# Kernel tuning notes

Measured on AMD Instinct MI355X. Metric: run time of the kernel, lower is better.

The kernel has to match this reference:

```python
import jax, jax.numpy as jnp
import numpy as np

N_HEAD = 16


def setup_inputs() -> dict:
    key = jax.random.key(0)
    ks = jax.random.split(key, 11)
    B, T, D = 8, 448, 1024
    init = 0.02
    x = jax.random.normal(ks[0], (B, T, D), dtype=jnp.float32)
    k_cache = jax.random.normal(ks[1], (B, T, D), dtype=jnp.float32)
    v_cache = jax.random.normal(ks[2], (B, T, D), dtype=jnp.float32)
    # Whisper-style additive causal mask: 0 on/below diagonal, large negative above
    mask = jnp.triu(jnp.full((T, T), -1e9, dtype=jnp.float32), k=1)
    Wq = jax.random.normal(ks[3], (D, D), dtype=jnp.float32) * init
    bq = jax.random.normal(ks[4], (D,), dtype=jnp.float32) * init
    Wk = jax.random.normal(ks[5], (D, D), dtype=jnp.float32) * init  # key proj has no bias
    Wv = jax.random.normal(ks[6], (D, D), dtype=jnp.float32) * init
    bv = jax.random.normal(ks[7], (D,), dtype=jnp.float32) * init
    Wo = jax.random.normal(ks[8], (D, D), dtype=jnp.float32) * init
    bo = jax.random.normal(ks[9], (D,), dtype=jnp.float32) * init
    return {"x": x, "k_cache": k_cache, "v_cache": v_cache, "mask": mask,
            "Wq": Wq, "bq": bq, "Wk": Wk, "Wv": Wv, "bv": bv, "Wo": Wo, "bo": bo}


def reference(x, k_cache, v_cache, mask, Wq, bq, Wk, Wv, bv, Wo, bo):
    # QKV projections (key has no bias, as in Whisper)
    q = x @ Wq + bq
    k = x @ Wk
    v = x @ Wv + bv
    # In-place KV cache append: write new keys/values into the tail of the cache
    T_new = k.shape[1]
    k_cache = k_cache.at[:, -T_new:, :].set(k)
    v_cache = v_cache.at[:, -T_new:, :].set(v)

    B, T, D = q.shape
    H = N_HEAD
    dh = D // H
    scale = dh ** (-0.25)  # applied to BOTH q and k

    qh = (q * scale).reshape(B, T, H, dh).transpose(0, 2, 1, 3)           # [B,H,T,dh]
    kh = (k_cache * scale).reshape(B, k_cache.shape[1], H, dh).transpose(0, 2, 1, 3)
    vh = v_cache.reshape(B, v_cache.shape[1], H, dh).transpose(0, 2, 1, 3)

    qk = jnp.einsum('bhqd,bhkd->bhqk', qh, kh) + mask[:T, :T]             # [B,H,T,Tc]
    qk = qk.astype(jnp.float32)  # upcast for softmax, matching original
    w = jax.nn.softmax(qk, axis=-1).astype(q.dtype)

    out = jnp.einsum('bhqk,bhkd->bhqd', w, vh)                            # [B,H,T,dh]
    out = out.transpose(0, 2, 1, 3).reshape(B, T, D)
    return out @ Wo + bo, k_cache, v_cache
```

## Files before the change

kernel.cpp:

```cpp
#include <hip/hip_runtime.h>
#include <hip/hip_bf16.h>
#include <math.h>

#define B 8
#define T 448
#define D 1024
#define H 16
#define DH 64
#define M (B*T)

typedef short short8 __attribute__((ext_vector_type(8)));
typedef float floatx4 __attribute__((ext_vector_type(4)));
typedef unsigned short u16;

__device__ __forceinline__ u16 f2bf(float f) {
    union { float f; unsigned u; } v; v.f = f;
    unsigned r = v.u + 0x7FFF + ((v.u >> 16) & 1);
    return (u16)(r >> 16);
}

__device__ __forceinline__ void gload16(const void* gptr, void* lptr) {
    __builtin_amdgcn_global_load_lds(
        (const __attribute__((address_space(1))) void*)gptr,
        (__attribute__((address_space(3))) void*)lptr, 16, 0, 0);
}

__global__ __launch_bounds__(256) void xconv(const float* __restrict__ x, u16* __restrict__ xb) {
    const int i = blockIdx.x * 256 + threadIdx.x;
    float4 v = ((const float4*)x)[i];
    ushort4 o;
    o.x = f2bf(v.x); o.y = f2bf(v.y); o.z = f2bf(v.z); o.w = f2bf(v.w);
    ((ushort4*)xb)[i] = o;
}

__global__ __launch_bounds__(256) void wconv4(
    const float* __restrict__ Wq, const float* __restrict__ Wk,
    const float* __restrict__ Wv, const float* __restrict__ Wo,
    u16* __restrict__ wt)
{
    __shared__ float tile[64][65];
    const int z = blockIdx.z;
    const float* W = (z == 0) ? Wq : (z == 1) ? Wk : (z == 2) ? Wv : Wo;
    u16* Wt = wt + (size_t)z * D * D;
    const int k0 = blockIdx.y * 64, n0 = blockIdx.x * 64;
    const int tr = threadIdx.x >> 4, tc = threadIdx.x & 15;
    #pragma unroll
    for (int i = 0; i < 4; ++i) {
        float4 v = *(const float4*)(W + (size_t)(k0 + tr + 16 * i) * D + n0 + tc * 4);
        tile[tr + 16 * i][tc * 4 + 0] = v.x;
        tile[tr + 16 * i][tc * 4 + 1] = v.y;
        tile[tr + 16 * i][tc * 4 + 2] = v.z;
        tile[tr + 16 * i][tc * 4 + 3] = v.w;
    }
    __syncthreads();
    #pragma unroll
    for (int i = 0; i < 4; ++i) {
        const int n = tr + 16 * i;
        ushort4 o;
        o.x = f2bf(tile[tc * 4 + 0][n]);
        o.y = f2bf(tile[tc * 4 + 1][n]);
        o.z = f2bf(tile[tc * 4 + 2][n]);
        o.w = f2bf(tile[tc * 4 + 3][n]);
        *(ushort4*)(Wt + (size_t)(n0 + n) * D + k0 + tc * 4) = o;
    }
}

__global__ __launch_bounds__(256) void gemm128(
    const u16* __restrict__ A, const u16* __restrict__ Bt, int mode,
    const float* __restrict__ bq, const float* __restrict__ bv,
    u16* __restrict__ qkvb, float* __restrict__ kout, float* __restrict__ vout,
    u16* __restrict__ vbT,
    const float* __restrict__ bo, float* __restrict__ outp)
{
    __shared__ u16 As[2][128][32];
    __shared__ u16 Bs[2][128][32];
    const int m0 = blockIdx.y * 128;
    const int n0 = blockIdx.x * 128;
    const int tid = threadIdx.x;
    const int wave = tid >> 6, lane = tid & 63;
    const int wy = wave >> 1, wx = wave & 1;
    const int lrow = lane & 15, lquad = lane >> 4;

    floatx4 acc[4][4];
    #pragma unroll
    for (int i = 0; i < 4; ++i)
        #pragma unroll
        for (int j = 0; j < 4; ++j)
            acc[i][j] = (floatx4){0.f, 0.f, 0.f, 0.f};

    const u16* agp0 = A + (size_t)(m0 + (tid >> 2)) * 1024 + (tid & 3) * 8;
    const u16* agp1 = agp0 + (size_t)64 * 1024;
    const u16* bgp0 = Bt + (size_t)(n0 + (tid >> 2)) * 1024 + (tid & 3) * 8;
    const u16* bgp1 = bgp0 + (size_t)64 * 1024;
    char* lA[2] = { (char*)&As[0][0][0] + wave * 1024, (char*)&As[1][0][0] + wave * 1024 };
    char* lB[2] = { (char*)&Bs[0][0][0] + wave * 1024, (char*)&Bs[1][0][0] + wave * 1024 };

    gload16(agp0, lA[0]);
    gload16(agp1, lA[0] + 4096);
    gload16(bgp0, lB[0]);
    gload16(bgp1, lB[0] + 4096);

    for (int it = 0; it < 32; ++it) {
        const int cur = it & 1;
        __syncthreads();
        if (it < 31) {
            const int k = (it + 1) * 32;
            const int nx = cur ^ 1;
            gload16(agp0 + k, lA[nx]);
            gload16(agp1 + k, lA[nx] + 4096);
            gload16(bgp0 + k, lB[nx]);
            gload16(bgp1 + k, lB[nx] + 4096);
        }
        short8 af[4], bfr[4];
        #pragma unroll
        for (int i = 0; i < 4; ++i)
            af[i] = *(const short8*)&As[cur][wy * 64 + i * 16 + lrow][lquad * 8];
        #pragma unroll
        for (int j = 0; j < 4; ++j)
            bfr[j] = *(const short8*)&Bs[cur][wx * 64 + j * 16 + lrow][lquad * 8];
        #pragma unroll
        for (int i = 0; i < 4; ++i)
            #pragma unroll
            for (int j = 0; j < 4; ++j)
                acc[i][j] = __builtin_amdgcn_mfma_f32_16x16x32_bf16(af[i], bfr[j], acc[i][j], 0, 0, 0);
    }

    const int sec = (mode == 0) ? (n0 >> 10) : 3;
    #pragma unroll
    for (int j = 0; j < 4; ++j) {
        const int col = n0 + wx * 64 + j * 16 + lrow;
        float bb;
        if (mode == 1) bb = bo[col];
        else bb = (sec == 0) ? bq[col] : (sec == 2 ? bv[col - 2048] : 0.f);
        #pragma unroll
        for (int i = 0; i < 4; ++i) {
            #pragma unroll
            for (int r = 0; r < 4; ++r) {
                const int row = m0 + wy * 64 + i * 16 + lquad * 4 + r;
                const float v = acc[i][j][r] + bb;
                if (mode == 1) {
                    outp[(size_t)row * 1024 + col] = v;
                } else if (sec == 0) {
                    qkvb[(size_t)row * 3072 + col] = f2bf(v);
                } else if (sec == 1) {
                    qkvb[(size_t)row * 3072 + col] = f2bf(v);
                    kout[(size_t)row * 1024 + col - 1024] = v;
                } else {
                    vout[(size_t)row * 1024 + col - 2048] = v;
                    const int bidx = row / 448, tt = row - bidx * 448;
                    vbT[((size_t)bidx * 1024 + (col - 2048)) * 448 + tt] = f2bf(v);
                }
            }
        }
    }
}

__global__ __launch_bounds__(256) void flash_attn(
    const u16* __restrict__ QKVb,
    const u16* __restrict__ VbT,
    u16* __restrict__ Ob)
{
    __shared__ u16 Qs[64][72];
    __shared__ u16 Ks[64][72];
    __shared__ u16 Vt[64][72];
    __shared__ u16 Pt[4][16][72];
    const int qt = blockIdx.x;
    const int bh = blockIdx.y;
    const int h = bh & (H - 1), b = bh >> 4;
    const int tid = threadIdx.x, wave = tid >> 6, lane = tid & 63;
    const int lrow = lane & 15, lquad = lane >> 4;
    const int q0 = qt * 64;

    const u16* qbase = QKVb + (size_t)b * T * 3072 + (size_t)h * DH;
    const u16* kbase = qbase + 1024;
    const u16* vtb   = VbT + (size_t)bh * DH * T;

    {
        const int s = tid * 2;
        short8 v0 = *(const short8*)(qbase + (size_t)(q0 + (s >> 3)) * 3072 + (s & 7) * 8);
        short8 v1 = *(const short8*)(qbase + (size_t)(q0 + ((s + 1) >> 3)) * 3072 + ((s + 1) & 7) * 8);
        *(short8*)&Qs[s >> 3][(s & 7) * 8] = v0;
        *(short8*)&Qs[(s + 1) >> 3][((s + 1) & 7) * 8] = v1;
    }
    __syncthreads();
    short8 aq0 = *(const short8*)&Qs[wave * 16 + lrow][lquad * 8];
    short8 aq1 = *(const short8*)&Qs[wave * 16 + lrow][32 + lquad * 8];

    float m_i[4], l_i[4];
    floatx4 oacc[4];
    #pragma unroll
    for (int r = 0; r < 4; ++r) { m_i[r] = -INFINITY; l_i[r] = 0.f; }
    #pragma unroll
    for (int n = 0; n < 4; ++n) oacc[n] = (floatx4){0.f, 0.f, 0.f, 0.f};

    const float SC = 0.125f * 1.44269504088896340736f;
    const int nkt = qt + 1;

    for (int kt = 0; kt < nkt; ++kt) {
        const int k0 = kt * 64;
        {
            const int s = tid * 2;
            const int r0 = s >> 3, o0 = (s & 7) * 8;
            const int r1 = (s + 1) >> 3, o1 = ((s + 1) & 7) * 8;
            short8 kv0 = *(const short8*)(kbase + (size_t)(k0 + r0) * 3072 + o0);
            short8 kv1 = *(const short8*)(kbase + (size_t)(k0 + r1) * 3072 + o1);
            short8 vv0 = *(const short8*)(vtb + (size_t)r0 * T + k0 + o0);
            short8 vv1 = *(const short8*)(vtb + (size_t)r1 * T + k0 + o1);
            __syncthreads();
            *(short8*)&Ks[r0][o0] = kv0;
            *(short8*)&Ks[r1][o1] = kv1;
            *(short8*)&Vt[r0][o0] = vv0;
            *(short8*)&Vt[r1][o1] = vv1;
        }
        __syncthreads();

        floatx4 s4[4];
        #pragma unroll
        for (int sub = 0; sub < 4; ++sub) {
            short8 bk0 = *(const short8*)&Ks[sub * 16 + lrow][lquad * 8];
            short8 bk1 = *(const short8*)&Ks[sub * 16 + lrow][32 + lquad * 8];
            floatx4 z = (floatx4){0.f, 0.f, 0.f, 0.f};
            z = __builtin_amdgcn_mfma_f32_16x16x32_bf16(aq0, bk0, z, 0, 0, 0);
            z = __builtin_amdgcn_mfma_f32_16x16x32_bf16(aq1, bk1, z, 0, 0, 0);
            s4[sub] = z;
        }

        float p[4][4];
        #pragma unroll
        for (int r = 0; r < 4; ++r) {
            const int qg = q0 + wave * 16 + lquad * 4 + r;
            float sv[4];
            float mx = -INFINITY;
            #pragma unroll
            for (int sub = 0; sub < 4; ++sub) {
                const int kk = k0 + sub * 16 + lrow;
                float v = s4[sub][r] * SC;
                v = (kk <= qg) ? v : -INFINITY;
                sv[sub] = v;
                mx = fmaxf(mx, v);
            }
            mx = fmaxf(mx, __shfl_xor(mx, 1));
            mx = fmaxf(mx, __shfl_xor(mx, 2));
            mx = fmaxf(mx, __shfl_xor(mx, 4));
            mx = fmaxf(mx, __shfl_xor(mx, 8));
            const float mnew = fmaxf(m_i[r], mx);
            const float alpha = exp2f(m_i[r] - mnew);
            float ls = 0.f;
            #pragma unroll
            for (int sub = 0; sub < 4; ++sub) {
                const float pv = exp2f(sv[sub] - mnew);
                p[sub][r] = pv;
                ls += pv;
            }
            ls += __shfl_xor(ls, 1);
            ls += __shfl_xor(ls, 2);
            ls += __shfl_xor(ls, 4);
            ls += __shfl_xor(ls, 8);
            l_i[r] = l_i[r] * alpha + ls;
            m_i[r] = mnew;
            #pragma unroll
            for (int n = 0; n < 4; ++n) oacc[n][r] *= alpha;
        }

        #pragma unroll
        for (int sub = 0; sub < 4; ++sub)
            #pragma unroll
            for (int r = 0; r < 4; ++r)
                Pt[wave][lquad * 4 + r][sub * 16 + lrow] = f2bf(p[sub][r]);
        __syncthreads();
        short8 ap0 = *(const short8*)&Pt[wave][lrow][lquad * 8];
        short8 ap1 = *(const short8*)&Pt[wave][lrow][32 + lquad * 8];

        #pragma unroll
        for (int n = 0; n < 4; ++n) {
            short8 bv0 = *(const short8*)&Vt[n * 16 + lrow][lquad * 8];
            short8 bv1 = *(const short8*)&Vt[n * 16 + lrow][32 + lquad * 8];
            oacc[n] = __builtin_amdgcn_mfma_f32_16x16x32_bf16(ap0, bv0, oacc[n], 0, 0, 0);
            oacc[n] = __builtin_amdgcn_mfma_f32_16x16x32_bf16(ap1, bv1, oacc[n], 0, 0, 0);
        }
    }

    #pragma unroll
    for (int r = 0; r < 4; ++r) {
        const float inv = 1.f / l_i[r];
        const int qg = q0 + wave * 16 + lquad * 4 + r;
        u16* orow = Ob + ((size_t)b * T + qg) * D + (size_t)h * DH;
        #pragma unroll
        for (int n = 0; n < 4; ++n)
            orow[n * 16 + lrow] = f2bf(oacc[n][r] * inv);
    }
}

extern "C" void kernel_launch(void* const* d_in, const int* in_sizes, int n_in,
                              void* d_out, int out_size, void* d_ws, size_t ws_size,
                              hipStream_t stream) {
    const float* x  = (const float*)d_in[0];
    const float* Wq = (const float*)d_in[4];
    const float* bq = (const float*)d_in[5];
    const float* Wk = (const float*)d_in[6];
    const float* Wv = (const float*)d_in[7];
    const float* bv = (const float*)d_in[8];
    const float* Wo = (const float*)d_in[9];
    const float* bo = (const float*)d_in[10];

    float* out  = (float*)d_out;
    float* kout = out + (size_t)M * D;
    float* vout = out + 2 * (size_t)M * D;

    u16* xb   = (u16*)d_ws;
    u16* wt   = xb   + (size_t)M * D;
    u16* qkvb = wt   + (size_t)4 * D * D;
    u16* vbT  = qkvb + (size_t)M * 3 * D;
    u16* ab   = vbT  + (size_t)M * D;

    xconv<<<M * D / 1024, 256, 0, stream>>>(x, xb);
    wconv4<<<dim3(16, 16, 4), 256, 0, stream>>>(Wq, Wk, Wv, Wo, wt);

    gemm128<<<dim3(24, 28), 256, 0, stream>>>(xb, wt, 0, bq, bv,
                                              qkvb, kout, vout, vbT, nullptr, nullptr);

    flash_attn<<<dim3(7, 128), 256, 0, stream>>>(qkvb, vbT, ab);

    gemm128<<<dim3(8, 28), 256, 0, stream>>>(ab, wt + (size_t)3 * D * D, 1, nullptr, nullptr,
                                             nullptr, nullptr, nullptr, nullptr, bo, out);
}
```

Measured before the change: 206.5 us.

## Merge conversion kernels, XCD-aware GEMM tile mapping, 32-row flash attention tiles

Three separate changes. The x and weight conversion kernels are merged into one launch, saving a kernel launch. Both GEMMs switch to a flattened 1D grid that assigns neighbouring N tiles to the same XCD, so L2 reuse of weight tiles improves. Flash attention now uses 32-query tiles with 128-thread blocks, which doubles the block count and gives finer causal balance, at the cost of loading each K/V tile for twice as many blocks.

```diff
diff --git a/kernel.cpp b/kernel.cpp
--- a/kernel.cpp
+++ b/kernel.cpp
@@ -25,43 +25,51 @@
         (__attribute__((address_space(3))) void*)lptr, 16, 0, 0);
 }
 
-__global__ __launch_bounds__(256) void xconv(const float* __restrict__ x, u16* __restrict__ xb) {
-    const int i = blockIdx.x * 256 + threadIdx.x;
-    float4 v = ((const float4*)x)[i];
-    ushort4 o;
-    o.x = f2bf(v.x); o.y = f2bf(v.y); o.z = f2bf(v.z); o.w = f2bf(v.w);
-    ((ushort4*)xb)[i] = o;
-}
-
-__global__ __launch_bounds__(256) void wconv4(
+__global__ __launch_bounds__(256) void prep(
+    const float* __restrict__ x,
     const float* __restrict__ Wq, const float* __restrict__ Wk,
     const float* __restrict__ Wv, const float* __restrict__ Wo,
-    u16* __restrict__ wt)
+    u16* __restrict__ wt, u16* __restrict__ xb)
 {
     __shared__ float tile[64][65];
-    const int z = blockIdx.z;
-    const float* W = (z == 0) ? Wq : (z == 1) ? Wk : (z == 2) ? Wv : Wo;
-    u16* Wt = wt + (size_t)z * D * D;
-    const int k0 = blockIdx.y * 64, n0 = blockIdx.x * 64;
-    const int tr = threadIdx.x >> 4, tc = threadIdx.x & 15;
-    #pragma unroll
-    for (int i = 0; i < 4; ++i) {
-        float4 v = *(const float4*)(W + (size_t)(k0 + tr + 16 * i) * D + n0 + tc * 4);
-        tile[tr + 16 * i][tc * 4 + 0] = v.x;
-        tile[tr + 16 * i][tc * 4 + 1] = v.y;
-        tile[tr + 16 * i][tc * 4 + 2] = v.z;
-        tile[tr + 16 * i][tc * 4 + 3] = v.w;
-    }
-    __syncthreads();
-    #pragma unroll
-    for (int i = 0; i < 4; ++i) {
-        const int n = tr + 16 * i;
-        ushort4 o;
-        o.x = f2bf(tile[tc * 4 + 0][n]);
-        o.y = f2bf(tile[tc * 4 + 1][n]);
-        o.z = f2bf(tile[tc * 4 + 2][n]);
-        o.w = f2bf(tile[tc * 4 + 3][n]);
-        *(ushort4*)(Wt + (size_t)(n0 + n) * D + k0 + tc * 4) = o;
+    const int bid = blockIdx.x;
+    const int tid = threadIdx.x;
+    if (bid < 1024) {
+        const int z = bid >> 8;
+        const int t = bid & 255;
+        const float* W = (z == 0) ? Wq : (z == 1) ? Wk : (z == 2) ? Wv : Wo;
+        u16* Wt = wt + (size_t)z * D * D;
+        const int k0 = (t >> 4) * 64, n0 = (t & 15) * 64;
+        const int tr = tid >> 4, tc = tid & 15;
+        #pragma unroll
+        for (int i = 0; i < 4; ++i) {
+            float4 v = *(const float4*)(W + (size_t)(k0 + tr + 16 * i) * D + n0 + tc * 4);
+            tile[tr + 16 * i][tc * 4 + 0] = v.x;
+            tile[tr + 16 * i][tc * 4 + 1] = v.y;
+            tile[tr + 16 * i][tc * 4 + 2] = v.z;
+            tile[tr + 16 * i][tc * 4 + 3] = v.w;
+        }
+        __syncthreads();
+        #pragma unroll
+        for (int i = 0; i < 4; ++i) {
+            const int n = tr + 16 * i;
+            ushort4 o;
+            o.x = f2bf(tile[tc * 4 + 0][n]);
+            o.y = f2bf(tile[tc * 4 + 1][n]);
+            o.z = f2bf(tile[tc * 4 + 2][n]);
+            o.w = f2bf(tile[tc * 4 + 3][n]);
+            *(ushort4*)(Wt + (size_t)(n0 + n) * D + k0 + tc * 4) = o;
+        }
+    } else {
+        const size_t base = (size_t)(bid - 1024) * 4096;
+        #pragma unroll
+        for (int j = 0; j < 4; ++j) {
+            const size_t idx = base + (size_t)(j * 256 + tid) * 4;
+            float4 v = *(const float4*)(x + idx);
+            ushort4 o;
+            o.x = f2bf(v.x); o.y = f2bf(v.y); o.z = f2bf(v.z); o.w = f2bf(v.w);
+            *(ushort4*)(xb + idx) = o;
+        }
     }
 }
 
@@ -74,8 +82,13 @@
 {
     __shared__ u16 As[2][128][32];
     __shared__ u16 Bs[2][128][32];
-    const int m0 = blockIdx.y * 128;
-    const int n0 = blockIdx.x * 128;
+    const int flat = blockIdx.x;
+    const int xcd = flat & 7, local = flat >> 3;
+    int mt, nt;
+    if (mode == 0) { nt = xcd * 3 + (local % 3); mt = local / 3; }
+    else           { nt = xcd;                   mt = local;      }
+    const int m0 = mt * 128;
+    const int n0 = nt * 128;
     const int tid = threadIdx.x;
     const int wave = tid >> 6, lane = tid & 63;
     const int wy = wave >> 1, wx = wave & 1;
@@ -155,21 +168,21 @@
     }
 }
 
-__global__ __launch_bounds__(256) void flash_attn(
+__global__ __launch_bounds__(128) void flash_attn(
     const u16* __restrict__ QKVb,
     const u16* __restrict__ VbT,
     u16* __restrict__ Ob)
 {
-    __shared__ u16 Qs[64][72];
+    __shared__ u16 Qs[32][72];
     __shared__ u16 Ks[64][72];
     __shared__ u16 Vt[64][72];
-    __shared__ u16 Pt[4][16][72];
+    __shared__ u16 Pt[2][16][72];
     const int qt = blockIdx.x;
     const int bh = blockIdx.y;
     const int h = bh & (H - 1), b = bh >> 4;
     const int tid = threadIdx.x, wave = tid >> 6, lane = tid & 63;
     const int lrow = lane & 15, lquad = lane >> 4;
-    const int q0 = qt * 64;
+    const int q0 = qt * 32;
 
     const u16* qbase = QKVb + (size_t)b * T * 3072 + (size_t)h * DH;
     const u16* kbase = qbase + 1024;
@@ -194,23 +207,26 @@
     for (int n = 0; n < 4; ++n) oacc[n] = (floatx4){0.f, 0.f, 0.f, 0.f};
 
     const float SC = 0.125f * 1.44269504088896340736f;
-    const int nkt = qt + 1;
+    const int nkt = ((qt * 32 + 31) >> 6) + 1;
 
     for (int kt = 0; kt < nkt; ++kt) {
         const int k0 = kt * 64;
         {
-            const int s = tid * 2;
-            const int r0 = s >> 3, o0 = (s & 7) * 8;
-            const int r1 = (s + 1) >> 3, o1 = ((s + 1) & 7) * 8;
-            short8 kv0 = *(const short8*)(kbase + (size_t)(k0 + r0) * 3072 + o0);
-            short8 kv1 = *(const short8*)(kbase + (size_t)(k0 + r1) * 3072 + o1);
-            short8 vv0 = *(const short8*)(vtb + (size_t)r0 * T + k0 + o0);
-            short8 vv1 = *(const short8*)(vtb + (size_t)r1 * T + k0 + o1);
+            short8 kv[4], vv[4];
+            int rr[4], oo[4];
+            #pragma unroll
+            for (int c = 0; c < 4; ++c) {
+                const int s = tid * 4 + c;
+                rr[c] = s >> 3; oo[c] = (s & 7) * 8;
+                kv[c] = *(const short8*)(kbase + (size_t)(k0 + rr[c]) * 3072 + oo[c]);
+                vv[c] = *(const short8*)(vtb + (size_t)rr[c] * T + k0 + oo[c]);
+            }
             __syncthreads();
-            *(short8*)&Ks[r0][o0] = kv0;
-            *(short8*)&Ks[r1][o1] = kv1;
-            *(short8*)&Vt[r0][o0] = vv0;
-            *(short8*)&Vt[r1][o1] = vv1;
+            #pragma unroll
+            for (int c = 0; c < 4; ++c) {
+                *(short8*)&Ks[rr[c]][oo[c]] = kv[c];
+                *(short8*)&Vt[rr[c]][oo[c]] = vv[c];
+            }
         }
         __syncthreads();
 
@@ -313,14 +329,13 @@
     u16* vbT  = qkvb + (size_t)M * 3 * D;
     u16* ab   = vbT  + (size_t)M * D;
 
-    xconv<<<M * D / 1024, 256, 0, stream>>>(x, xb);
-    wconv4<<<dim3(16, 16, 4), 256, 0, stream>>>(Wq, Wk, Wv, Wo, wt);
-
-    gemm128<<<dim3(24, 28), 256, 0, stream>>>(xb, wt, 0, bq, bv,
-                                              qkvb, kout, vout, vbT, nullptr, nullptr);
-
-    flash_attn<<<dim3(7, 128), 256, 0, stream>>>(qkvb, vbT, ab);
-
-    gemm128<<<dim3(8, 28), 256, 0, stream>>>(ab, wt + (size_t)3 * D * D, 1, nullptr, nullptr,
-                                             nullptr, nullptr, nullptr, nullptr, bo, out);
-}
+    prep<<<1920, 256, 0, stream>>>(x, Wq, Wk, Wv, Wo, wt, xb);
+
+    gemm128<<<672, 256, 0, stream>>>(xb, wt, 0, bq, bv,
+                                     qkvb, kout, vout, vbT, nullptr, nullptr);
+
+    flash_attn<<<dim3(14, 128), 128, 0, stream>>>(qkvb, vbT, ab);
+
+    gemm128<<<224, 256, 0, stream>>>(ab, wt + (size_t)3 * D * D, 1, nullptr, nullptr,
+                                     nullptr, nullptr, nullptr, nullptr, bo, out);
+}
```

New measurement: 220.0 us. 1.07x slower.
